# Kernel optimization log

Measured on AMD Instinct MI355X. Metric: run time of the kernel, lower is better.

Reference implementation:

```python
import jax, jax.numpy as jnp
import numpy as np

B, H, W = 64, 84, 84
IN_F, HID, NCLS = 128, 256, 50
C2 = IN_F * 2  # 256
EPS = 1e-5
K_NEIGH = 4


def _ring_edges(batch):
    rows = np.repeat(np.arange(batch), K_NEIGH)
    offs = np.tile(np.arange(1, K_NEIGH + 1), batch)
    cols = (rows + offs) % batch
    return jnp.asarray(np.stack([rows, cols]), dtype=jnp.int32)


def setup_inputs() -> dict:
    key = jax.random.key(0)
    ks = jax.random.split(key, 40)
    i = iter(range(40))
    def n(shape, s=0.05):
        return jax.random.normal(ks[next(i)], shape, jnp.float32) * s
    def u(shape):
        return jax.random.uniform(ks[next(i)], shape, jnp.float32, 0.5, 1.5)
    d = {}
    d['x'] = jax.random.normal(ks[next(i)], (B, 3, H, W), jnp.float32)
    # conv1 + bn1
    d['conv1_w'] = n((IN_F, 3, 3, 3)); d['conv1_b'] = n((IN_F,))
    d['bn1_g'] = 1.0 + n((IN_F,)); d['bn1_b'] = n((IN_F,))
    d['bn1_m'] = n((IN_F,)); d['bn1_v'] = u((IN_F,))
    # conv2 + bn2
    d['conv2_w'] = n((C2, IN_F, 3, 3)); d['conv2_b'] = n((C2,))
    d['bn2_g'] = 1.0 + n((C2,)); d['bn2_b'] = n((C2,))
    d['bn2_m'] = n((C2,)); d['bn2_v'] = u((C2,))
    # conv3 + bn3
    d['conv3_w'] = n((C2, C2, 3, 3)); d['conv3_b'] = n((C2,))
    d['bn3_g'] = 1.0 + n((C2,)); d['bn3_b'] = n((C2,))
    d['bn3_m'] = n((C2,)); d['bn3_v'] = u((C2,))
    # gcn1: Linear(256,256), attn Linear(512,1)
    d['gcn1_lw'] = n((HID, C2)); d['gcn1_lb'] = n((HID,))
    d['gcn1_aw'] = n((1, 2 * C2)); d['gcn1_ab'] = n((1,))
    # gcn2: Linear(256,256), attn Linear(512,1)
    d['gcn2_lw'] = n((HID, HID)); d['gcn2_lb'] = n((HID,))
    d['gcn2_aw'] = n((1, 2 * HID)); d['gcn2_ab'] = n((1,))
    # fc
    d['fc_w'] = n((NCLS, HID)); d['fc_b'] = n((NCLS,))
    d['edge_index'] = _ring_edges(B)  # [2, 4*B] deterministic ring graph
    return d


def _conv_bn_relu(x, w, b, g, be, m, v):
    y = jax.lax.conv_general_dilated(
        x, w, window_strides=(1, 1), padding='SAME',
        dimension_numbers=('NCHW', 'OIHW', 'NCHW')) + b[None, :, None, None]
    scale = (g / jnp.sqrt(v + EPS))[None, :, None, None]
    y = (y - m[None, :, None, None]) * scale + be[None, :, None, None]
    return jax.nn.relu(y)


def _gcn_conv(h, row, col, lw, lb, aw, ab):
    # h: [N, F]; edge gather -> attn MLP -> global softmax -> scatter-add
    ef = jnp.concatenate([h[row], h[col]], axis=1)          # [E, 2F]
    ew = jax.nn.leaky_relu(ef @ aw.T + ab, 0.01)            # [E, 1]
    ew = jax.nn.softmax(ew, axis=0)                          # softmax over all edges
    agg = jnp.zeros_like(h).at[row].add(h[col] * ew)        # [N, F]
    return agg @ lw.T + lb + h                               # linear + residual


def reference(x, conv1_w, conv1_b, bn1_g, bn1_b, bn1_m, bn1_v,
              conv2_w, conv2_b, bn2_g, bn2_b, bn2_m, bn2_v,
              conv3_w, conv3_b, bn3_g, bn3_b, bn3_m, bn3_v,
              gcn1_lw, gcn1_lb, gcn1_aw, gcn1_ab,
              gcn2_lw, gcn2_lb, gcn2_aw, gcn2_ab,
              fc_w, fc_b, edge_index):
    h = _conv_bn_relu(x, conv1_w, conv1_b, bn1_g, bn1_b, bn1_m, bn1_v)
    h = _conv_bn_relu(h, conv2_w, conv2_b, bn2_g, bn2_b, bn2_m, bn2_v)
    h = _conv_bn_relu(h, conv3_w, conv3_b, bn3_g, bn3_b, bn3_m, bn3_v)
    h = h.mean(axis=(2, 3))                                  # adaptive avg pool 1x1 + flatten -> [B, 256]
    row, col = edge_index[0], edge_index[1]
    h = jax.nn.relu(_gcn_conv(h, row, col, gcn1_lw, gcn1_lb, gcn1_aw, gcn1_ab))
    h = jax.nn.relu(_gcn_conv(h, row, col, gcn2_lw, gcn2_lb, gcn2_aw, gcn2_ab))
    return h @ fc_w.T + fc_b                                 # [B, 50]
```

## Files before the change

kernel.cpp:

```cpp
#include <hip/hip_runtime.h>
#include <hip/hip_bf16.h>

typedef __attribute__((ext_vector_type(8))) short bf16x8;
typedef __attribute__((ext_vector_type(4))) float f32x4;

#define DEV __device__ __forceinline__

static constexpr int Bn   = 64;
static constexpr int Hs   = 84;
static constexpr int HP   = 86;
static constexpr int C1c  = 128;
static constexpr int C2c  = 256;
static constexpr int NPOS = Hs * Hs;
static constexpr float EPSf = 1e-5f;

DEV __hip_bfloat16 f2b(float v) { return __float2bfloat16(v); }

DEV void gload16(const void* g, void* l) {
    __builtin_amdgcn_global_load_lds(
        (const __attribute__((address_space(1))) void*)g,
        (__attribute__((address_space(3))) void*)l, 16, 0, 0);
}

__global__ __launch_bounds__(128) void conv1_k(
    const float* __restrict__ x,
    const float* __restrict__ w,  const float* __restrict__ cb,
    const float* __restrict__ g,  const float* __restrict__ be,
    const float* __restrict__ mm, const float* __restrict__ vv,
    __hip_bfloat16* __restrict__ h1)
{
    __shared__ float xin[3][3][HP];
    int bi = blockIdx.x;
    int b = bi / Hs, y = bi % Hs;
    int t = threadIdx.x;

    for (int idx = t; idx < 3 * 3 * HP; idx += 128) {
        int ci = idx / (3 * HP);
        int r  = idx % (3 * HP);
        int dy = r / HP;
        int xx = r % HP;
        int iy = y + dy - 1;
        int ix = xx - 1;
        float v = 0.f;
        if (iy >= 0 && iy < Hs && ix >= 0 && ix < Hs)
            v = x[((size_t)(b * 3 + ci) * Hs + iy) * Hs + ix];
        xin[ci][dy][xx] = v;
    }
    int co = t;
    float wr[3][3][3];
    for (int ci = 0; ci < 3; ci++)
        for (int dy = 0; dy < 3; dy++)
            for (int dx = 0; dx < 3; dx++)
                wr[ci][dy][dx] = w[((co * 3 + ci) * 3 + dy) * 3 + dx];
    float scale = g[co] / sqrtf(vv[co] + EPSf);
    float bias  = (cb[co] - mm[co]) * scale + be[co];
    __syncthreads();

    for (int xp = 0; xp < Hs; xp++) {
        float acc = 0.f;
        #pragma unroll
        for (int ci = 0; ci < 3; ci++)
            #pragma unroll
            for (int dy = 0; dy < 3; dy++)
                #pragma unroll
                for (int dx = 0; dx < 3; dx++)
                    acc += xin[ci][dy][xp + dx] * wr[ci][dy][dx];
        float o = acc * scale + bias;
        o = o > 0.f ? o : 0.f;
        h1[((size_t)(b * HP + y + 1) * HP + (xp + 1)) * C1c + co] = f2b(o);
    }
}

template <int C>
__global__ void halo_zero(__hip_bfloat16* __restrict__ h)
{
    int i = blockIdx.x;
    int b = i / 340, p = i % 340;
    int y, xx;
    if (p < 86)       { y = 0;  xx = p; }
    else if (p < 172) { y = 85; xx = p - 86; }
    else if (p < 256) { xx = 0; y = p - 172 + 1; }
    else              { xx = 85; y = p - 256 + 1; }
    h[((size_t)(b * HP + y) * HP + xx) * C + threadIdx.x] = f2b(0.f);
}

template <int CIN>
__global__ void prep_w(const float* __restrict__ w, __hip_bfloat16* __restrict__ wm)
{
    int e  = blockIdx.x * 256 + threadIdx.x;
    int k  = e >> 8;
    int co = e & 255;
    int tap = k / CIN;
    int ci  = k % CIN;
    int ty = tap / 3, tx = tap % 3;
    wm[(size_t)(k >> 5) * 8192 + co * 32 + (k & 31)] =
        f2b(w[((size_t)(co * CIN + ci) * 3 + ty) * 3 + tx]);
}

__global__ void prep_sb(const float* __restrict__ cb, const float* __restrict__ g,
                        const float* __restrict__ be, const float* __restrict__ mm,
                        const float* __restrict__ vv, float* __restrict__ sb)
{
    int co = threadIdx.x;
    float s = g[co] / sqrtf(vv[co] + EPSf);
    sb[co] = s;
    sb[256 + co] = (cb[co] - mm[co]) * s + be[co];
}

__global__ void zero_f32(float* __restrict__ p)
{
    p[blockIdx.x * 256 + threadIdx.x] = 0.f;
}

template <int CIN, bool POOL>
__global__ __launch_bounds__(256, 2) void conv_igemm(
    const __hip_bfloat16* __restrict__ in, const __hip_bfloat16* __restrict__ wgt,
    const float* __restrict__ sb, __hip_bfloat16* __restrict__ out, float* __restrict__ pool)
{
    constexpr int KB = CIN / 32;
    constexpr int NT = 9 * KB;
    __shared__ __align__(16) unsigned short As[3 * 128 * 32];
    __shared__ __align__(16) unsigned short Bs[3 * 256 * 32];
    __shared__ float pl[512];

    int t = threadIdx.x;
    int l = t & 63, w = t >> 6;
    int lidx = l & 15, lg = l >> 4;
    int wm = w >> 1, wn = w & 1;

    int nwg  = (int)gridDim.x;
    int orig = (int)blockIdx.x;
    int xcd = orig & 7, idx = orig >> 3;
    int q = nwg >> 3, r = nwg & 7;
    int bx = (xcd < r ? xcd * (q + 1) : r * (q + 1) + (xcd - r) * q) + idx;
    int m0 = bx * 128;

    int sseg = (l & 3) ^ ((l >> 3) & 3);
    int srow = w * 16 + (l >> 2);
    const __hip_bfloat16 *pA0, *pA1, *pB0, *pB1, *pB2, *pB3;
    {
        int gm0 = m0 + srow;
        int b0 = gm0 / NPOS; int r0 = gm0 - b0 * NPOS; int y0 = r0 / Hs; int x0 = r0 - y0 * Hs;
        pA0 = in + ((size_t)(b0 * HP + y0) * HP + x0) * CIN + sseg * 8;
        int gm1 = m0 + srow + 64;
        int b1 = gm1 / NPOS; int r1 = gm1 - b1 * NPOS; int y1 = r1 / Hs; int x1 = r1 - y1 * Hs;
        pA1 = in + ((size_t)(b1 * HP + y1) * HP + x1) * CIN + sseg * 8;
        pB0 = wgt + (size_t)(srow      ) * 32 + sseg * 8;
        pB1 = wgt + (size_t)(srow +  64) * 32 + sseg * 8;
        pB2 = wgt + (size_t)(srow + 128) * 32 + sseg * 8;
        pB3 = wgt + (size_t)(srow + 192) * 32 + sseg * 8;
    }
    char* AsB = (char*)As;
    char* BsB = (char*)Bs;

    int swz = (lidx >> 1) & 3;
    unsigned aLane = (unsigned)((wm * 64  + lidx) * 64 + ((lg ^ swz) * 16));
    unsigned bLane = (unsigned)((wn * 128 + lidx) * 64 + ((lg ^ swz) * 16));

    f32x4 acc[4][8];
    #pragma unroll
    for (int m = 0; m < 4; m++)
        #pragma unroll
        for (int n = 0; n < 8; n++)
            acc[m][n] = (f32x4){0.f, 0.f, 0.f, 0.f};
    if (POOL) { pl[t] = 0.f; pl[256 + t] = 0.f; }

    auto ISSUE = [&](int s, unsigned cA, unsigned cB) {
        int kb = s / 9, tap = s - kb * 9;
        int ty = tap / 3, tx = tap - ty * 3;
        size_t aoff = (size_t)(ty * HP + tx) * CIN + kb * 32;
        size_t boff = (size_t)(tap * KB + kb) * 8192;
        gload16(pA0 + aoff, AsB + cA + w * 1024);
        gload16(pA1 + aoff, AsB + cA + w * 1024 + 4096);
        gload16(pB0 + boff, BsB + cB + w * 1024);
        gload16(pB1 + boff, BsB + cB + w * 1024 + 4096);
        gload16(pB2 + boff, BsB + cB + w * 1024 + 8192);
        gload16(pB3 + boff, BsB + cB + w * 1024 + 12288);
    };

    auto COMP = [&](unsigned cA, unsigned cB) {
        bf16x8 av[4]; bf16x8 bv[8];
        #pragma unroll
        for (int m = 0; m < 4; m++)
            av[m] = *(const bf16x8*)(AsB + cA + aLane + m * 1024);
        #pragma unroll
        for (int n = 0; n < 8; n++)
            bv[n] = *(const bf16x8*)(BsB + cB + bLane + n * 1024);
        __builtin_amdgcn_s_setprio(1);
        #pragma unroll
        for (int m = 0; m < 4; m++)
            #pragma unroll
            for (int n = 0; n < 8; n++)
                acc[m][n] = __builtin_amdgcn_mfma_f32_16x16x32_bf16(av[m], bv[n], acc[m][n], 0, 0, 0);
        __builtin_amdgcn_s_setprio(0);
    };

    ISSUE(0, 0u, 0u);
    ISSUE(1, 8192u, 16384u);

    unsigned cA0 = 0u,     cB0 = 0u;
    unsigned cA1 = 8192u,  cB1 = 16384u;
    unsigned cA2 = 16384u, cB2 = 32768u;
    for (int kt = 0; kt < NT - 1; ++kt) {
        asm volatile("s_waitcnt vmcnt(6) lgkmcnt(0)" ::: "memory");
        __builtin_amdgcn_s_barrier();
        asm volatile("" ::: "memory");
        if (kt + 2 < NT) ISSUE(kt + 2, cA2, cB2);
        COMP(cA0, cB0);
        unsigned ta = cA0, tb = cB0;
        cA0 = cA1; cB0 = cB1;
        cA1 = cA2; cB1 = cB2;
        cA2 = ta;  cB2 = tb;
    }
    asm volatile("s_waitcnt vmcnt(0) lgkmcnt(0)" ::: "memory");
    __builtin_amdgcn_s_barrier();
    asm volatile("" ::: "memory");
    COMP(cA0, cB0);

    float sc[8], bi2[8];
    #pragma unroll
    for (int n = 0; n < 8; n++) {
        int cn = wn * 128 + n * 16 + lidx;
        sc[n]  = sb[cn];
        bi2[n] = sb[256 + cn];
    }

    if (!POOL) {
        #pragma unroll
        for (int m = 0; m < 4; m++) {
            #pragma unroll
            for (int r2 = 0; r2 < 4; r2++) {
                int row = wm * 64 + m * 16 + lg * 4 + r2;
                int gm2 = m0 + row;
                int b2  = gm2 / NPOS;
                int rm2 = gm2 - b2 * NPOS;
                int y2  = rm2 / Hs;
                int x2  = rm2 - y2 * Hs;
                size_t ob = ((size_t)(b2 * HP + y2 + 1) * HP + (x2 + 1)) * 256;
                #pragma unroll
                for (int n = 0; n < 8; n++) {
                    float v = acc[m][n][r2] * sc[n] + bi2[n];
                    v = v > 0.f ? v : 0.f;
                    out[ob + wn * 128 + n * 16 + lidx] = f2b(v);
                }
            }
        }
    } else {
        int bs_lo   = m0 / NPOS;
        int row_lim = (bs_lo + 1) * NPOS - m0;
        #pragma unroll
        for (int n = 0; n < 8; n++) {
            float s0 = 0.f, s1 = 0.f;
            #pragma unroll
            for (int m = 0; m < 4; m++)
                #pragma unroll
                for (int r2 = 0; r2 < 4; r2++) {
                    int row = wm * 64 + m * 16 + lg * 4 + r2;
                    float v = acc[m][n][r2] * sc[n] + bi2[n];
                    v = v > 0.f ? v : 0.f;
                    if (row < row_lim) s0 += v; else s1 += v;
                }
            int cl = wn * 128 + n * 16 + lidx;
            atomicAdd(&pl[cl], s0);
            if (row_lim < 128) atomicAdd(&pl[256 + cl], s1);
        }
        __syncthreads();
        atomicAdd(&pool[bs_lo * 256 + t], pl[t]);
        if (row_lim < 128) atomicAdd(&pool[(bs_lo + 1) * 256 + t], pl[256 + t]);
    }
}

__global__ void pool_div(const float* __restrict__ pool, float* __restrict__ h0)
{
    int i = blockIdx.x * 256 + threadIdx.x;
    h0[i] = pool[i] * (1.0f / (float)NPOS);
}

__global__ __launch_bounds__(256) void gcn_attn(
    const float* __restrict__ h, const float* __restrict__ aw,
    const float* __restrict__ ab, const int* __restrict__ ei,
    float* __restrict__ ew)
{
    __shared__ float p[64], q[64], red[256];
    int t = threadIdx.x;
    if (t < 64) {
        float pp = 0.f, qq = 0.f;
        for (int c = 0; c < 256; c++) {
            float hv = h[t * 256 + c];
            pp += hv * aw[c];
            qq += hv * aw[256 + c];
        }
        p[t] = pp; q[t] = qq;
    }
    __syncthreads();
    int r = ei[t], c = ei[256 + t];
    float s = p[r] + q[c] + ab[0];
    s = s >= 0.f ? s : 0.01f * s;
    red[t] = s;
    __syncthreads();
    for (int st = 128; st > 0; st >>= 1) {
        if (t < st) red[t] = fmaxf(red[t], red[t + st]);
        __syncthreads();
    }
    float mx = red[0];
    __syncthreads();
    float e = expf(s - mx);
    red[t] = e;
    __syncthreads();
    for (int st = 128; st > 0; st >>= 1) {
        if (t < st) red[t] += red[t + st];
        __syncthreads();
    }
    ew[t] = e / red[0];
}

__global__ __launch_bounds__(256) void gcn_agg(
    const float* __restrict__ h, const float* __restrict__ ew, const int* __restrict__ ei,
    const float* __restrict__ lw, const float* __restrict__ lb,
    float* __restrict__ ho)
{
    __shared__ float agg[256];
    __shared__ float ewl[256];
    __shared__ int rl[256], cl[256];
    int n = blockIdx.x;
    int t = threadIdx.x;
    ewl[t] = ew[t];
    rl[t] = ei[t];
    cl[t] = ei[256 + t];
    __syncthreads();
    float a = 0.f;
    for (int e = 0; e < 256; e++)
        if (rl[e] == n) a += ewl[e] * h[cl[e] * 256 + t];
    agg[t] = a;
    __syncthreads();
    float o = 0.f;
    for (int c2 = 0; c2 < 256; c2++)
        o += agg[c2] * lw[t * 256 + c2];
    o += lb[t] + h[n * 256 + t];
    o = o > 0.f ? o : 0.f;
    ho[n * 256 + t] = o;
}

__global__ void fc_k(const float* __restrict__ h, const float* __restrict__ fw,
                     const float* __restrict__ fb, float* __restrict__ out)
{
    int n = blockIdx.x;
    int t = threadIdx.x;
    if (t < 50) {
        float o = 0.f;
        for (int c = 0; c < 256; c++)
            o += h[n * 256 + c] * fw[t * 256 + c];
        o += fb[t];
        out[n * 50 + t] = o;
    }
}

extern "C" void kernel_launch(void* const* d_in, const int* in_sizes, int n_in,
                              void* d_out, int out_size, void* d_ws, size_t ws_size,
                              hipStream_t stream)
{
    (void)in_sizes; (void)n_in; (void)out_size;

    const float* X    = (const float*)d_in[0];
    const float* c1w  = (const float*)d_in[1];
    const float* c1b  = (const float*)d_in[2];
    const float* b1g  = (const float*)d_in[3];
    const float* b1b  = (const float*)d_in[4];
    const float* b1m  = (const float*)d_in[5];
    const float* b1v  = (const float*)d_in[6];
    const float* c2w  = (const float*)d_in[7];
    const float* c2b  = (const float*)d_in[8];
    const float* b2g  = (const float*)d_in[9];
    const float* b2b  = (const float*)d_in[10];
    const float* b2m  = (const float*)d_in[11];
    const float* b2v  = (const float*)d_in[12];
    const float* c3w  = (const float*)d_in[13];
    const float* c3b  = (const float*)d_in[14];
    const float* b3g  = (const float*)d_in[15];
    const float* b3b  = (const float*)d_in[16];
    const float* b3m  = (const float*)d_in[17];
    const float* b3v  = (const float*)d_in[18];
    const float* g1lw = (const float*)d_in[19];
    const float* g1lb = (const float*)d_in[20];
    const float* g1aw = (const float*)d_in[21];
    const float* g1ab = (const float*)d_in[22];
    const float* g2lw = (const float*)d_in[23];
    const float* g2lb = (const float*)d_in[24];
    const float* g2aw = (const float*)d_in[25];
    const float* g2ab = (const float*)d_in[26];
    const float* fcw  = (const float*)d_in[27];
    const float* fcb  = (const float*)d_in[28];
    const int*   EI   = (const int*)d_in[29];

    size_t fixedB = 3000000;
    int chb = 8;
    if (ws_size >= (size_t)64 * 5680128 + fixedB)      chb = 64;
    else if (ws_size >= (size_t)32 * 5680128 + fixedB) chb = 32;
    else if (ws_size >= (size_t)16 * 5680128 + fixedB) chb = 16;
    int nchunks = Bn / chb;
    int mch = chb * NPOS;

    char* p = (char*)d_ws;
    auto carve = [&](size_t bytes) {
        char* r = p;
        p += (bytes + 255) & ~(size_t)255;
        return r;
    };
    __hip_bfloat16* h1c = (__hip_bfloat16*)carve((size_t)chb * HP * HP * C1c * 2);
    __hip_bfloat16* h2c = (__hip_bfloat16*)carve((size_t)chb * HP * HP * C2c * 2);
    __hip_bfloat16* wm2 = (__hip_bfloat16*)carve((size_t)9 * C1c * 256 * 2);
    __hip_bfloat16* wm3 = (__hip_bfloat16*)carve((size_t)9 * C2c * 256 * 2);
    float* sb2  = (float*)carve(512 * 4);
    float* sb3  = (float*)carve(512 * 4);
    float* pool = (float*)carve(64 * 256 * 4);
    float* h0   = (float*)carve(64 * 256 * 4);
    float* hg1  = (float*)carve(64 * 256 * 4);
    float* hg2  = (float*)carve(64 * 256 * 4);
    float* ew1  = (float*)carve(256 * 4);
    float* ew2  = (float*)carve(256 * 4);

    halo_zero<C1c><<<dim3(chb * 340), dim3(C1c), 0, stream>>>(h1c);
    halo_zero<C2c><<<dim3(chb * 340), dim3(C2c), 0, stream>>>(h2c);
    prep_w<C1c><<<dim3(9 * C1c), dim3(256), 0, stream>>>(c2w, wm2);
    prep_w<C2c><<<dim3(9 * C2c), dim3(256), 0, stream>>>(c3w, wm3);
    prep_sb<<<dim3(1), dim3(256), 0, stream>>>(c2b, b2g, b2b, b2m, b2v, sb2);
    prep_sb<<<dim3(1), dim3(256), 0, stream>>>(c3b, b3g, b3b, b3m, b3v, sb3);
    zero_f32<<<dim3(64), dim3(256), 0, stream>>>(pool);

    for (int ch = 0; ch < nchunks; ch++) {
        const float* xch = X + (size_t)ch * chb * 3 * NPOS;
        conv1_k<<<dim3(chb * Hs), dim3(C1c), 0, stream>>>(
            xch, c1w, c1b, b1g, b1b, b1m, b1v, h1c);
        conv_igemm<C1c, false><<<dim3(mch / 128), dim3(256), 0, stream>>>(
            h1c, wm2, sb2, h2c, nullptr);
        conv_igemm<C2c, true ><<<dim3(mch / 128), dim3(256), 0, stream>>>(
            h2c, wm3, sb3, nullptr, pool + (size_t)ch * chb * 256);
    }
    pool_div<<<dim3(64), dim3(256), 0, stream>>>(pool, h0);

    gcn_attn<<<dim3(1), dim3(256), 0, stream>>>(h0, g1aw, g1ab, EI, ew1);
    gcn_agg<<<dim3(64), dim3(256), 0, stream>>>(h0, ew1, EI, g1lw, g1lb, hg1);
    gcn_attn<<<dim3(1), dim3(256), 0, stream>>>(hg1, g2aw, g2ab, EI, ew2);
    gcn_agg<<<dim3(64), dim3(256), 0, stream>>>(hg1, ew2, EI, g2lw, g2lb, hg2);
    fc_k<<<dim3(64), dim3(64), 0, stream>>>(hg2, fcw, fcb, (float*)d_out);
}
```

Measured before the change: 1.048 ms.

## Load A operand straight from global into registers and double-buffer B in LDS

The im2col A tile no longer goes through shared memory. Each wave now loads its A fragments from global memory directly into registers, using per-row pointers computed once. The B (weight) tile pipeline goes from a triple-buffered LDS ring to a double buffer with an unrolled two-stage loop, and A registers are ping-ponged between two sets. This removes the A LDS traffic and shrinks LDS use. In exchange, A is fetched redundantly by the two N-waves, global load latency is exposed directly to the MFMA operands, and prefetch depth drops from two stages to one.

Result: slower. 1.172 ms (+11.8%).

```diff
diff --git a/kernel.cpp b/kernel.cpp
--- a/kernel.cpp
+++ b/kernel.cpp
@@ -119,8 +119,7 @@
 {
     constexpr int KB = CIN / 32;
     constexpr int NT = 9 * KB;
-    __shared__ __align__(16) unsigned short As[3 * 128 * 32];
-    __shared__ __align__(16) unsigned short Bs[3 * 256 * 32];
+    __shared__ __align__(16) unsigned short Bs[2 * 256 * 32];
     __shared__ float pl[512];
 
     int t = threadIdx.x;
@@ -137,52 +136,50 @@
 
     int sseg = (l & 3) ^ ((l >> 3) & 3);
     int srow = w * 16 + (l >> 2);
-    const __hip_bfloat16 *pA0, *pA1, *pB0, *pB1, *pB2, *pB3;
-    {
-        int gm0 = m0 + srow;
-        int b0 = gm0 / NPOS; int r0 = gm0 - b0 * NPOS; int y0 = r0 / Hs; int x0 = r0 - y0 * Hs;
-        pA0 = in + ((size_t)(b0 * HP + y0) * HP + x0) * CIN + sseg * 8;
-        int gm1 = m0 + srow + 64;
-        int b1 = gm1 / NPOS; int r1 = gm1 - b1 * NPOS; int y1 = r1 / Hs; int x1 = r1 - y1 * Hs;
-        pA1 = in + ((size_t)(b1 * HP + y1) * HP + x1) * CIN + sseg * 8;
-        pB0 = wgt + (size_t)(srow      ) * 32 + sseg * 8;
-        pB1 = wgt + (size_t)(srow +  64) * 32 + sseg * 8;
-        pB2 = wgt + (size_t)(srow + 128) * 32 + sseg * 8;
-        pB3 = wgt + (size_t)(srow + 192) * 32 + sseg * 8;
-    }
-    char* AsB = (char*)As;
+    const __hip_bfloat16* pB0 = wgt + (size_t)(srow      ) * 32 + sseg * 8;
+    const __hip_bfloat16* pB1 = wgt + (size_t)(srow +  64) * 32 + sseg * 8;
+    const __hip_bfloat16* pB2 = wgt + (size_t)(srow + 128) * 32 + sseg * 8;
+    const __hip_bfloat16* pB3 = wgt + (size_t)(srow + 192) * 32 + sseg * 8;
     char* BsB = (char*)Bs;
 
     int swz = (lidx >> 1) & 3;
-    unsigned aLane = (unsigned)((wm * 64  + lidx) * 64 + ((lg ^ swz) * 16));
     unsigned bLane = (unsigned)((wn * 128 + lidx) * 64 + ((lg ^ swz) * 16));
+
+    const __hip_bfloat16* pAr[4];
+    #pragma unroll
+    for (int m = 0; m < 4; m++) {
+        int gm = m0 + wm * 64 + m * 16 + lidx;
+        int b0 = gm / NPOS; int r0 = gm - b0 * NPOS;
+        int y0 = r0 / Hs;   int x0 = r0 - y0 * Hs;
+        pAr[m] = in + ((size_t)(b0 * HP + y0) * HP + x0) * CIN + lg * 8;
+    }
 
     f32x4 acc[4][8];
     #pragma unroll
-    for (int m = 0; m < 4; m++)
-        #pragma unroll
-        for (int n = 0; n < 8; n++)
-            acc[m][n] = (f32x4){0.f, 0.f, 0.f, 0.f};
+    for (int i = 0; i < 4; i++)
+        #pragma unroll
+        for (int j = 0; j < 8; j++)
+            acc[i][j] = (f32x4){0.f, 0.f, 0.f, 0.f};
     if (POOL) { pl[t] = 0.f; pl[256 + t] = 0.f; }
 
-    auto ISSUE = [&](int s, unsigned cA, unsigned cB) {
+    auto ISSUE_B = [&](int s, unsigned cB) {
         int kb = s / 9, tap = s - kb * 9;
-        int ty = tap / 3, tx = tap - ty * 3;
-        size_t aoff = (size_t)(ty * HP + tx) * CIN + kb * 32;
         size_t boff = (size_t)(tap * KB + kb) * 8192;
-        gload16(pA0 + aoff, AsB + cA + w * 1024);
-        gload16(pA1 + aoff, AsB + cA + w * 1024 + 4096);
         gload16(pB0 + boff, BsB + cB + w * 1024);
         gload16(pB1 + boff, BsB + cB + w * 1024 + 4096);
         gload16(pB2 + boff, BsB + cB + w * 1024 + 8192);
         gload16(pB3 + boff, BsB + cB + w * 1024 + 12288);
     };
-
-    auto COMP = [&](unsigned cA, unsigned cB) {
-        bf16x8 av[4]; bf16x8 bv[8];
+    auto LOAD_A = [&](int s, bf16x8 (&aw)[4]) {
+        int kb = s / 9, tap = s - kb * 9;
+        int ty = tap / 3, tx = tap - ty * 3;
+        int aoff = (ty * HP + tx) * CIN + kb * 32;
         #pragma unroll
         for (int m = 0; m < 4; m++)
-            av[m] = *(const bf16x8*)(AsB + cA + aLane + m * 1024);
+            aw[m] = *(const bf16x8*)(pAr[m] + aoff);
+    };
+    auto COMP = [&](unsigned cB, const bf16x8 (&aw)[4]) {
+        bf16x8 bv[8];
         #pragma unroll
         for (int n = 0; n < 8; n++)
             bv[n] = *(const bf16x8*)(BsB + cB + bLane + n * 1024);
@@ -191,31 +188,38 @@
         for (int m = 0; m < 4; m++)
             #pragma unroll
             for (int n = 0; n < 8; n++)
-                acc[m][n] = __builtin_amdgcn_mfma_f32_16x16x32_bf16(av[m], bv[n], acc[m][n], 0, 0, 0);
+                acc[m][n] = __builtin_amdgcn_mfma_f32_16x16x32_bf16(aw[m], bv[n], acc[m][n], 0, 0, 0);
         __builtin_amdgcn_s_setprio(0);
     };
 
-    ISSUE(0, 0u, 0u);
-    ISSUE(1, 8192u, 16384u);
-
-    unsigned cA0 = 0u,     cB0 = 0u;
-    unsigned cA1 = 8192u,  cB1 = 16384u;
-    unsigned cA2 = 16384u, cB2 = 32768u;
-    for (int kt = 0; kt < NT - 1; ++kt) {
-        asm volatile("s_waitcnt vmcnt(6) lgkmcnt(0)" ::: "memory");
+    bf16x8 aA[4], aB[4];
+    ISSUE_B(0, 0u);
+    __builtin_amdgcn_sched_barrier(0);
+    LOAD_A(0, aA);
+    __builtin_amdgcn_sched_barrier(0);
+
+    for (int kt = 0; kt < NT; kt += 2) {
+        asm volatile("s_waitcnt vmcnt(4) lgkmcnt(0)" ::: "memory");
         __builtin_amdgcn_s_barrier();
         asm volatile("" ::: "memory");
-        if (kt + 2 < NT) ISSUE(kt + 2, cA2, cB2);
-        COMP(cA0, cB0);
-        unsigned ta = cA0, tb = cB0;
-        cA0 = cA1; cB0 = cB1;
-        cA1 = cA2; cB1 = cB2;
-        cA2 = ta;  cB2 = tb;
-    }
-    asm volatile("s_waitcnt vmcnt(0) lgkmcnt(0)" ::: "memory");
-    __builtin_amdgcn_s_barrier();
-    asm volatile("" ::: "memory");
-    COMP(cA0, cB0);
+        if (kt + 1 < NT) {
+            ISSUE_B(kt + 1, 16384u);
+            __builtin_amdgcn_sched_barrier(0);
+            LOAD_A(kt + 1, aB);
+            __builtin_amdgcn_sched_barrier(0);
+        }
+        COMP(0u, aA);
+        asm volatile("s_waitcnt vmcnt(4) lgkmcnt(0)" ::: "memory");
+        __builtin_amdgcn_s_barrier();
+        asm volatile("" ::: "memory");
+        if (kt + 2 < NT) {
+            ISSUE_B(kt + 2, 0u);
+            __builtin_amdgcn_sched_barrier(0);
+            LOAD_A(kt + 2, aA);
+            __builtin_amdgcn_sched_barrier(0);
+        }
+        COMP(16384u, aB);
+    }
 
     float sc[8], bi2[8];
     #pragma unroll
```
